# Kernel optimization log

Measured on AMD Instinct MI355X. Metric: run time of the kernel, lower is better.

The kernel has to match this reference:

```python
import jax, jax.numpy as jnp
import numpy as np

_SQRT2 = 1.4142135623730951

def _norm_cdf(z):
    return 0.5 * (1.0 + jax.scipy.special.erf(z / _SQRT2))

def _cv_squared(v):
    # torch.var is unbiased (ddof=1)
    return jnp.var(v, ddof=1) / (jnp.mean(v) ** 2 + 1e-10)

def setup_inputs() -> dict:
    key = jax.random.key(0)
    ks = jax.random.split(key, 6)
    B, Cin, Cout, H, W, E = 64, 32, 32, 64, 64, 16
    return {
        "x": jax.random.normal(ks[0], (B, Cin, H, W), jnp.float32),
        "noise": jax.random.normal(ks[1], (B, E), jnp.float32),
        "w_gate": jax.random.normal(ks[2], (Cin, E), jnp.float32) * 0.1,
        "w_noise": jax.random.normal(ks[3], (Cin, E), jnp.float32) * 0.1,
        "expert_w": jax.random.normal(ks[4], (E, Cout, Cin, 3, 3), jnp.float32) * 0.05,
        "expert_b": jax.random.normal(ks[5], (E, Cout), jnp.float32) * 0.05,
    }

def _forward(x, noise, w_gate, w_noise, expert_w, expert_b, k=4, loss_coef=0.01, noise_eps=0.01):
    B = x.shape[0]
    # gate features: adaptive avg pool to 1x1 then flatten -> [B, Cin]
    gate_x = x.mean(axis=(2, 3))
    clean = gate_x @ w_gate                      # [B, E]
    std = jax.nn.softplus(gate_x @ w_noise) + noise_eps
    noisy = clean + noise * std                  # noisy logits (training path)
    logits = jax.nn.softmax(noisy, axis=1)       # NOTE: original softmaxes before top-k
    top_logits, top_idx = jax.lax.top_k(logits, k + 1)
    top_k_logits = top_logits[:, :k]
    top_k_idx = top_idx[:, :k]
    top_k_gates = top_k_logits / (top_k_logits.sum(1, keepdims=True) + 1e-6)
    gates = jnp.zeros_like(logits).at[jnp.arange(B)[:, None], top_k_idx].set(top_k_gates)
    # _prob_in_top_k: thresholds come from the post-softmax top values,
    # compared against pre-softmax clean/noisy logits (faithful to source)
    thr_in = top_logits[:, k:k + 1]
    thr_out = top_logits[:, k - 1:k]
    prob = jnp.where(noisy > thr_in,
                     _norm_cdf((clean - thr_in) / std),
                     _norm_cdf((clean - thr_out) / std))
    load = prob.sum(0)
    importance = gates.sum(0)
    loss = (_cv_squared(importance) + _cv_squared(load)) * loss_coef
    # dispatch/combine: since gates are exactly zero for unselected experts,
    # sum_e gates[:,e] * expert_e(x) equals SparseDispatcher's gather-compute-scatter.
    def step(acc, xs):
        w, b, g = xs  # w [Co,Ci,3,3], b [Co], g [B]
        out = jax.lax.conv_general_dilated(x, w, (1, 1), [(1, 1), (1, 1)])
        out = out + b[None, :, None, None]
        return acc + g[:, None, None, None] * out, None
    y0 = jnp.zeros((B, expert_w.shape[1], x.shape[2], x.shape[3]), x.dtype)
    y, _ = jax.lax.scan(step, y0, (expert_w, expert_b, gates.T))
    return y, loss

def reference(x, noise, w_gate, w_noise, expert_w, expert_b):
    return _forward(x, noise, w_gate, w_noise, expert_w, expert_b)
```

## Files before the change

### kernel.cpp

```cpp
#include <hip/hip_runtime.h>
#include <math.h>

#define B 64
#define CIN 32
#define COUT 32
#define E 16
#define TOPK 4

typedef __attribute__((ext_vector_type(8))) short short8;
typedef __attribute__((ext_vector_type(4))) float f32x4;

__device__ __forceinline__ unsigned short f2bf(float f) {
    unsigned int u = __float_as_uint(f);
    u += 0x7fffu + ((u >> 16) & 1u);
    return (unsigned short)(u >> 16);
}

__device__ __forceinline__ int swz1024(int o) { return (o & 7) * 128 + (o >> 3); }
__device__ __forceinline__ int swz256(int o)  { return (o & 7) * 32  + (o >> 3); }

__device__ __forceinline__ int cswz(int wp, int c) {
    return c ^ (((wp >> 2) & 3) << 3);
}

__global__ void __launch_bounds__(256)
bandsum_kernel(const float* __restrict__ x, float* __restrict__ bandsum) {
    int blk = swz1024(blockIdx.x);
    int b = blk >> 4, band = blk & 15, h0 = band << 2;
    int t = threadIdx.x, wave = t >> 6, l = t & 63;
    const float4* x4 = reinterpret_cast<const float4*>(x);

    float racc[8];
    #pragma unroll
    for (int k = 0; k < 8; k++) {
        int c = k * 4 + wave;
        float4 v = x4[(((size_t)(b * 32 + c) * 64 + h0 + (l >> 4)) << 4) + (l & 15)];
        racc[k] = (v.x + v.y) + (v.z + v.w);
    }
    #pragma unroll
    for (int off = 1; off < 64; off <<= 1)
        #pragma unroll
        for (int k = 0; k < 8; k++) racc[k] += __shfl_xor(racc[k], off, 64);
    if (l == 0) {
        #pragma unroll
        for (int k = 0; k < 8; k++)
            bandsum[((size_t)b * 16 + band) * 32 + k * 4 + wave] = racc[k];
    }
}

__global__ void __launch_bounds__(256)
gate_combine(const float* __restrict__ bandsum,
             const float* __restrict__ noise,
             const float* __restrict__ w_gate,
             const float* __restrict__ w_noise,
             const float* __restrict__ expert_w,
             const float* __restrict__ expert_b,
             unsigned short* __restrict__ cwb,
             float* __restrict__ cbias,
             float* __restrict__ probw,
             float* __restrict__ gimpw) {
    int blk = swz256(blockIdx.x);
    int b = blk >> 2, q = blk & 3;
    int t = threadIdx.x;

    __shared__ float gx[32];
    __shared__ float s_clean[E], s_std[E], s_noisy[E], s_lg[E];
    __shared__ float s_tv[TOPK + 1], s_g[TOPK];
    __shared__ int   s_gi[TOPK];

    if (t < 32) {
        const float* bp = bandsum + (size_t)b * 16 * 32 + t;
        float s = 0.f;
        #pragma unroll
        for (int j = 0; j < 16; j++) s += bp[j * 32];
        gx[t] = s * (1.f / 4096.f);
    }
    __syncthreads();
    if (t < E) {
        float s1 = 0.f, s2 = 0.f;
        #pragma unroll
        for (int c = 0; c < CIN; c++) {
            float g = gx[c];
            s1 += g * w_gate[c * E + t];
            s2 += g * w_noise[c * E + t];
        }
        float sp = fmaxf(s2, 0.f) + log1pf(expf(-fabsf(s2)));
        s_clean[t] = s1;
        s_std[t]   = sp + 0.01f;
        s_noisy[t] = s1 + noise[b * E + t] * (sp + 0.01f);
    }
    __syncthreads();
    if (t < E) {
        float m = s_noisy[0];
        #pragma unroll
        for (int e = 1; e < E; e++) m = fmaxf(m, s_noisy[e]);
        float den = 0.f;
        #pragma unroll
        for (int e = 0; e < E; e++) den += expf(s_noisy[e] - m);
        s_lg[t] = expf(s_noisy[t] - m) / den;
    }
    __syncthreads();
    if (t < E) {
        float v = s_lg[t]; int rank = 0;
        #pragma unroll
        for (int j = 0; j < E; j++) {
            float u = s_lg[j];
            rank += (u > v) || (u == v && j < t);
        }
        if (rank <= TOPK) s_tv[rank] = v;
        if (rank <  TOPK) s_gi[rank] = t;
    }
    __syncthreads();
    if (t < TOPK) {
        float s4 = s_tv[0] + s_tv[1] + s_tv[2] + s_tv[3] + 1e-6f;
        s_g[t] = s_tv[t] / s4;
    }
    __syncthreads();

    if (q == 0 && t < E) {
        float s4 = s_tv[0] + s_tv[1] + s_tv[2] + s_tv[3] + 1e-6f;
        float v = s_lg[t]; int rank = 0;
        #pragma unroll
        for (int j = 0; j < E; j++) {
            float u = s_lg[j];
            rank += (u > v) || (u == v && j < t);
        }
        gimpw[b * E + t] = (rank < TOPK) ? v / s4 : 0.f;
        const float INV_SQRT2 = 0.70710678118654752f;
        float thr_in = s_tv[TOPK], thr_out = s_tv[TOPK - 1];
        float thr = (s_noisy[t] > thr_in) ? thr_in : thr_out;
        float z = (s_clean[t] - thr) / s_std[t];
        probw[b * E + t] = 0.5f * (1.f + erff(z * INV_SQRT2));
    }
    if (q == 0 && t < COUT) {
        cbias[b * COUT + t] = s_g[0] * expert_b[s_gi[0] * 32 + t] + s_g[1] * expert_b[s_gi[1] * 32 + t]
                            + s_g[2] * expert_b[s_gi[2] * 32 + t] + s_g[3] * expert_b[s_gi[3] * 32 + t];
    }

    const float* e0 = expert_w + s_gi[0] * 9216;
    const float* e1 = expert_w + s_gi[1] * 9216;
    const float* e2 = expert_w + s_gi[2] * 9216;
    const float* e3 = expert_w + s_gi[3] * 9216;
    float g0 = s_g[0], g1 = s_g[1], g2 = s_g[2], g3 = s_g[3];
    #pragma unroll
    for (int k = 0; k < 9; k++) {
        int i = q * 2304 + k * 256 + t;
        int tap = i >> 10, cc = i & 1023;
        int rd = cc * 9 + tap;
        float s = g0 * e0[rd] + g1 * e1[rd] + g2 * e2[rd] + g3 * e3[rd];
        cwb[(size_t)b * 9216 + i] = f2bf(s);
    }
}

__global__ void __launch_bounds__(256)
conv_mfma(const float* __restrict__ x,
          const unsigned short* __restrict__ cwb,
          const float* __restrict__ cbias,
          const float* __restrict__ probw,
          const float* __restrict__ gimpw,
          float* __restrict__ y,
          float* __restrict__ loss_out) {
    int blk = swz1024(blockIdx.x);
    int b = blk >> 4, band = blk & 15, h0 = band << 2;
    int t = threadIdx.x, wave = t >> 6, l = t & 63;
    int ln = l & 15, lk = l >> 4;

    __shared__ unsigned short sx[6 * 66 * 32];

    const float4* x4 = reinterpret_cast<const float4*>(x);
    #pragma unroll
    for (int k = 0; k < 12; k++) {
        int i = k * 256 + t;
        int rr = i >> 9, c = (i >> 4) & 31, w4 = i & 15;
        int gr = h0 - 1 + rr;
        float4 v = {0.f, 0.f, 0.f, 0.f};
        if ((unsigned)gr < 64u)
            v = x4[(((size_t)(b * 32 + c) * 64 + gr) << 4) + w4];
        float vv[4] = {v.x, v.y, v.z, v.w};
        #pragma unroll
        for (int j = 0; j < 4; j++) {
            int wp = 1 + w4 * 4 + j;
            sx[(rr * 66 + wp) * 32 + cswz(wp, c)] = f2bf(vv[j]);
        }
    }
    for (int i = t; i < 384; i += 256) {
        int rr = i >> 6, rem = i & 63, side = rem >> 5, c = rem & 31;
        sx[(rr * 66 + side * 65) * 32 + c] = 0;
    }

    const unsigned short* wbase = cwb + (size_t)b * 9216;
    short8 afrag[2][9];
    #pragma unroll
    for (int tap = 0; tap < 9; tap++)
        #pragma unroll
        for (int ch = 0; ch < 2; ch++)
            afrag[ch][tap] = *reinterpret_cast<const short8*>(
                wbase + tap * 1024 + (ch * 16 + ln) * 32 + lk * 8);

    float bias0[4], bias1[4];
    #pragma unroll
    for (int r = 0; r < 4; r++) {
        bias0[r] = cbias[b * COUT + lk * 4 + r];
        bias1[r] = cbias[b * COUT + 16 + lk * 4 + r];
    }
    __syncthreads();

    int h = h0 + wave;
    for (int tile = 0; tile < 4; tile++) {
        int w0 = tile * 16;
        f32x4 acc0 = {0.f, 0.f, 0.f, 0.f};
        f32x4 acc1 = {0.f, 0.f, 0.f, 0.f};
        #pragma unroll
        for (int kh = 0; kh < 3; kh++) {
            int rr = wave + kh;
            #pragma unroll
            for (int kw = 0; kw < 3; kw++) {
                int wp = w0 + ln + kw;
                short8 bfrag = *reinterpret_cast<const short8*>(
                    &sx[(rr * 66 + wp) * 32 + cswz(wp, lk * 8)]);
                acc0 = __builtin_amdgcn_mfma_f32_16x16x32_bf16(afrag[0][kh * 3 + kw], bfrag, acc0, 0, 0, 0);
                acc1 = __builtin_amdgcn_mfma_f32_16x16x32_bf16(afrag[1][kh * 3 + kw], bfrag, acc1, 0, 0, 0);
            }
        }
        #pragma unroll
        for (int r = 0; r < 4; r++) {
            y[((size_t)(b * COUT + lk * 4 + r) * 64 + h) * 64 + w0 + ln]      = acc0[r] + bias0[r];
            y[((size_t)(b * COUT + 16 + lk * 4 + r) * 64 + h) * 64 + w0 + ln] = acc1[r] + bias1[r];
        }
    }

    if (blk == 0) {
        __shared__ float s_lv[32];
        if (t < 32) {
            const float* src = (t < 16) ? gimpw : probw;
            int e = t & 15;
            float s = 0.f;
            for (int bb = 0; bb < B; bb++) s += src[bb * E + e];
            s_lv[t] = s;
        }
        __syncthreads();
        if (t == 0) {
            float loss = 0.f;
            for (int pass = 0; pass < 2; pass++) {
                const float* v = s_lv + pass * 16;
                float mean = 0.f;
                for (int e = 0; e < E; e++) mean += v[e];
                mean *= (1.f / E);
                float var = 0.f;
                for (int e = 0; e < E; e++) { float d = v[e] - mean; var += d * d; }
                var *= (1.f / (E - 1));
                loss += var / (mean * mean + 1e-10f);
            }
            loss_out[0] = loss * 0.01f;
        }
    }
}

extern "C" void kernel_launch(void* const* d_in, const int* in_sizes, int n_in,
                              void* d_out, int out_size, void* d_ws, size_t ws_size,
                              hipStream_t stream) {
    const float* x        = (const float*)d_in[0];
    const float* noise    = (const float*)d_in[1];
    const float* w_gate   = (const float*)d_in[2];
    const float* w_noise  = (const float*)d_in[3];
    const float* expert_w = (const float*)d_in[4];
    const float* expert_b = (const float*)d_in[5];

    float* y    = (float*)d_out;
    float* loss = y + (size_t)B * COUT * 64 * 64;

    char* ws = (char*)d_ws;
    float*          bands  = (float*)(ws);
    float*          probw  = (float*)(ws + 131072);
    float*          gimpw  = (float*)(ws + 135168);
    float*          cbias  = (float*)(ws + 139264);
    unsigned short* cwb    = (unsigned short*)(ws + 147456);

    bandsum_kernel<<<B * 16, 256, 0, stream>>>(x, bands);
    gate_combine<<<256, 256, 0, stream>>>(bands, noise, w_gate, w_noise,
                                          expert_w, expert_b, cwb, cbias,
                                          probw, gimpw);
    conv_mfma<<<B * 16, 256, 0, stream>>>(x, cwb, cbias, probw, gimpw, y, loss);
}
```

Baseline: 32.88 us.

## Split gate_combine across more blocks with LDS-staged expert weights and shuffle softmax

```diff
diff --git a/kernel.cpp b/kernel.cpp
--- a/kernel.cpp
+++ b/kernel.cpp
@@ -17,7 +17,6 @@
 }
 
 __device__ __forceinline__ int swz1024(int o) { return (o & 7) * 128 + (o >> 3); }
-__device__ __forceinline__ int swz256(int o)  { return (o & 7) * 32  + (o >> 3); }
 
 __device__ __forceinline__ int cswz(int wp, int c) {
     return c ^ (((wp >> 2) & 3) << 3);
@@ -59,24 +58,39 @@
              float* __restrict__ cbias,
              float* __restrict__ probw,
              float* __restrict__ gimpw) {
-    int blk = swz256(blockIdx.x);
-    int b = blk >> 2, q = blk & 3;
+    int blk = swz1024(blockIdx.x);
+    int b = blk >> 4, s = blk & 15;
     int t = threadIdx.x;
 
+    __shared__ float elds[16 * 576];
     __shared__ float gx[32];
-    __shared__ float s_clean[E], s_std[E], s_noisy[E], s_lg[E];
     __shared__ float s_tv[TOPK + 1], s_g[TOPK];
     __shared__ int   s_gi[TOPK];
 
+    const float4* ew4 = reinterpret_cast<const float4*>(expert_w);
+    float4 stg[9];
+    #pragma unroll
+    for (int k = 0; k < 9; k++) {
+        int j = k * 256 + t;
+        int e = j / 144, off = j - e * 144;
+        stg[k] = ew4[(size_t)e * 2304 + s * 144 + off];
+    }
+
     if (t < 32) {
-        const float* bp = bandsum + (size_t)b * 16 * 32 + t;
-        float s = 0.f;
-        #pragma unroll
-        for (int j = 0; j < 16; j++) s += bp[j * 32];
-        gx[t] = s * (1.f / 4096.f);
-    }
-    __syncthreads();
-    if (t < E) {
+        const float* bp = bandsum + (size_t)b * 512 + t;
+        float acc = 0.f;
+        #pragma unroll
+        for (int j = 0; j < 16; j++) acc += bp[j * 32];
+        gx[t] = acc * (1.f / 4096.f);
+    }
+
+    #pragma unroll
+    for (int k = 0; k < 9; k++) {
+        int j = k * 256 + t;
+        *reinterpret_cast<float4*>(&elds[j * 4]) = stg[k];
+    }
+
+    if (t < 16) {
         float s1 = 0.f, s2 = 0.f;
         #pragma unroll
         for (int c = 0; c < CIN; c++) {
@@ -84,71 +98,53 @@
             s1 += g * w_gate[c * E + t];
             s2 += g * w_noise[c * E + t];
         }
-        float sp = fmaxf(s2, 0.f) + log1pf(expf(-fabsf(s2)));
-        s_clean[t] = s1;
-        s_std[t]   = sp + 0.01f;
-        s_noisy[t] = s1 + noise[b * E + t] * (sp + 0.01f);
+        float sp   = fmaxf(s2, 0.f) + log1pf(expf(-fabsf(s2)));
+        float stdv = sp + 0.01f;
+        float noisy = s1 + noise[b * E + t] * stdv;
+
+        float m = noisy;
+        #pragma unroll
+        for (int off = 1; off < 16; off <<= 1) m = fmaxf(m, __shfl_xor(m, off, 16));
+        float ex = expf(noisy - m);
+        float den = ex;
+        #pragma unroll
+        for (int off = 1; off < 16; off <<= 1) den += __shfl_xor(den, off, 16);
+        float lg = ex / den;
+
+        int rank = 0;
+        #pragma unroll
+        for (int j = 0; j < E; j++) {
+            float u = __shfl(lg, j, 16);
+            rank += (u > lg) || (u == lg && j < t);
+        }
+        if (rank <= TOPK) s_tv[rank] = lg;
+        if (rank <  TOPK) s_gi[rank] = t;
+        float s4 = s_tv[0] + s_tv[1] + s_tv[2] + s_tv[3] + 1e-6f;
+        if (rank < TOPK) s_g[rank] = lg / s4;
+
+        if (s == 0) {
+            gimpw[b * E + t] = (rank < TOPK) ? lg / s4 : 0.f;
+            const float INV_SQRT2 = 0.70710678118654752f;
+            float thr_in = s_tv[TOPK], thr_out = s_tv[TOPK - 1];
+            float thr = (noisy > thr_in) ? thr_in : thr_out;
+            float z = (s1 - thr) / stdv;
+            probw[b * E + t] = 0.5f * (1.f + erff(z * INV_SQRT2));
+        }
     }
     __syncthreads();
-    if (t < E) {
-        float m = s_noisy[0];
-        #pragma unroll
-        for (int e = 1; e < E; e++) m = fmaxf(m, s_noisy[e]);
-        float den = 0.f;
-        #pragma unroll
-        for (int e = 0; e < E; e++) den += expf(s_noisy[e] - m);
-        s_lg[t] = expf(s_noisy[t] - m) / den;
-    }
-    __syncthreads();
-    if (t < E) {
-        float v = s_lg[t]; int rank = 0;
-        #pragma unroll
-        for (int j = 0; j < E; j++) {
-            float u = s_lg[j];
-            rank += (u > v) || (u == v && j < t);
-        }
-        if (rank <= TOPK) s_tv[rank] = v;
-        if (rank <  TOPK) s_gi[rank] = t;
-    }
-    __syncthreads();
-    if (t < TOPK) {
-        float s4 = s_tv[0] + s_tv[1] + s_tv[2] + s_tv[3] + 1e-6f;
-        s_g[t] = s_tv[t] / s4;
-    }
-    __syncthreads();
-
-    if (q == 0 && t < E) {
-        float s4 = s_tv[0] + s_tv[1] + s_tv[2] + s_tv[3] + 1e-6f;
-        float v = s_lg[t]; int rank = 0;
-        #pragma unroll
-        for (int j = 0; j < E; j++) {
-            float u = s_lg[j];
-            rank += (u > v) || (u == v && j < t);
-        }
-        gimpw[b * E + t] = (rank < TOPK) ? v / s4 : 0.f;
-        const float INV_SQRT2 = 0.70710678118654752f;
-        float thr_in = s_tv[TOPK], thr_out = s_tv[TOPK - 1];
-        float thr = (s_noisy[t] > thr_in) ? thr_in : thr_out;
-        float z = (s_clean[t] - thr) / s_std[t];
-        probw[b * E + t] = 0.5f * (1.f + erff(z * INV_SQRT2));
-    }
-    if (q == 0 && t < COUT) {
-        cbias[b * COUT + t] = s_g[0] * expert_b[s_gi[0] * 32 + t] + s_g[1] * expert_b[s_gi[1] * 32 + t]
-                            + s_g[2] * expert_b[s_gi[2] * 32 + t] + s_g[3] * expert_b[s_gi[3] * 32 + t];
-    }
-
-    const float* e0 = expert_w + s_gi[0] * 9216;
-    const float* e1 = expert_w + s_gi[1] * 9216;
-    const float* e2 = expert_w + s_gi[2] * 9216;
-    const float* e3 = expert_w + s_gi[3] * 9216;
+
     float g0 = s_g[0], g1 = s_g[1], g2 = s_g[2], g3 = s_g[3];
-    #pragma unroll
-    for (int k = 0; k < 9; k++) {
-        int i = q * 2304 + k * 256 + t;
-        int tap = i >> 10, cc = i & 1023;
-        int rd = cc * 9 + tap;
-        float s = g0 * e0[rd] + g1 * e1[rd] + g2 * e2[rd] + g3 * e3[rd];
-        cwb[(size_t)b * 9216 + i] = f2bf(s);
+    int   i0 = s_gi[0], i1 = s_gi[1], i2 = s_gi[2], i3 = s_gi[3];
+    for (int local = t; local < 576; local += 256) {
+        int tap = local >> 6, ccl = local & 63;
+        int rdl = ccl * 9 + tap;
+        float v = g0 * elds[i0 * 576 + rdl] + g1 * elds[i1 * 576 + rdl]
+                + g2 * elds[i2 * 576 + rdl] + g3 * elds[i3 * 576 + rdl];
+        cwb[(size_t)b * 9216 + tap * 1024 + s * 64 + ccl] = f2bf(v);
+    }
+    if (s == 0 && t < COUT) {
+        cbias[b * COUT + t] = g0 * expert_b[i0 * 32 + t] + g1 * expert_b[i1 * 32 + t]
+                            + g2 * expert_b[i2 * 32 + t] + g3 * expert_b[i3 * 32 + t];
     }
 }
 
@@ -167,6 +163,21 @@
 
     __shared__ unsigned short sx[6 * 66 * 32];
 
+    const unsigned short* wbase = cwb + (size_t)b * 9216;
+    short8 afrag[2][9];
+    #pragma unroll
+    for (int tap = 0; tap < 9; tap++)
+        #pragma unroll
+        for (int ch = 0; ch < 2; ch++)
+            afrag[ch][tap] = *reinterpret_cast<const short8*>(
+                wbase + tap * 1024 + (ch * 16 + ln) * 32 + lk * 8);
+    float bias0[4], bias1[4];
+    #pragma unroll
+    for (int r = 0; r < 4; r++) {
+        bias0[r] = cbias[b * COUT + lk * 4 + r];
+        bias1[r] = cbias[b * COUT + 16 + lk * 4 + r];
+    }
+
     const float4* x4 = reinterpret_cast<const float4*>(x);
     #pragma unroll
     for (int k = 0; k < 12; k++) {
@@ -186,22 +197,6 @@
     for (int i = t; i < 384; i += 256) {
         int rr = i >> 6, rem = i & 63, side = rem >> 5, c = rem & 31;
         sx[(rr * 66 + side * 65) * 32 + c] = 0;
-    }
-
-    const unsigned short* wbase = cwb + (size_t)b * 9216;
-    short8 afrag[2][9];
-    #pragma unroll
-    for (int tap = 0; tap < 9; tap++)
-        #pragma unroll
-        for (int ch = 0; ch < 2; ch++)
-            afrag[ch][tap] = *reinterpret_cast<const short8*>(
-                wbase + tap * 1024 + (ch * 16 + ln) * 32 + lk * 8);
-
-    float bias0[4], bias1[4];
-    #pragma unroll
-    for (int r = 0; r < 4; r++) {
-        bias0[r] = cbias[b * COUT + lk * 4 + r];
-        bias1[r] = cbias[b * COUT + 16 + lk * 4 + r];
     }
     __syncthreads();
 
@@ -277,8 +272,8 @@
     unsigned short* cwb    = (unsigned short*)(ws + 147456);
 
     bandsum_kernel<<<B * 16, 256, 0, stream>>>(x, bands);
-    gate_combine<<<256, 256, 0, stream>>>(bands, noise, w_gate, w_noise,
-                                          expert_w, expert_b, cwb, cbias,
-                                          probw, gimpw);
+    gate_combine<<<B * 16, 256, 0, stream>>>(bands, noise, w_gate, w_noise,
+                                             expert_w, expert_b, cwb, cbias,
+                                             probw, gimpw);
     conv_mfma<<<B * 16, 256, 0, stream>>>(x, cwb, cbias, probw, gimpw, y, loss);
 }
```

After: 33.80 us. 2.8% more time.
